# Kernel optimization log

Hardware: AMD Instinct MI355X
Metric: run time of the kernel (lower is better)

## Reference

```python
import jax, jax.numpy as jnp
import numpy as np

COUNTS = [1536, 8192, 16384, 24576, 12288, 1024, 512, 512, 256, 128, 128]
OFFS = np.concatenate([[0], np.cumsum(COUNTS)]).astype(int).tolist()
N = OFFS[-1]          # 65536 atoms total, sorted by degree
MAX_DEG = 10
BATCH = 2048          # fixed GraphGather batch size
F_IN = 75
GC = 256
DENSE = 512
N_TASKS = 12
N_CLASSES = 2
BN_EPS = 1e-3         # keras BatchNormalization default epsilon


def _graph_conv(x, deg_adjs, w0, wself, wneigh, b):
    # deepchem GraphConv: per-degree (self @ Wself + sum_neighbors @ Wneigh + b), relu
    outs = [x[OFFS[0]:OFFS[1]] @ w0 + b[0]]  # degree-0 atoms: self transform only
    for d in range(1, MAX_DEG + 1):
        self_atoms = x[OFFS[d]:OFFS[d + 1]]            # [n_d, F]
        neigh = x[deg_adjs[d - 1]].sum(axis=1)         # gather [n_d, d, F] -> sum -> [n_d, F]
        outs.append(self_atoms @ wself[d - 1] + neigh @ wneigh[d - 1] + b[d])
    return jax.nn.relu(jnp.concatenate(outs, axis=0))


def _graph_pool(x, deg_adjs):
    # deepchem GraphPool: elementwise max over {self} U neighbors, per degree
    outs = [x[OFFS[0]:OFFS[1]]]  # degree-0 atoms pass through
    for d in range(1, MAX_DEG + 1):
        self_atoms = x[OFFS[d]:OFFS[d + 1]]
        outs.append(jnp.maximum(self_atoms, x[deg_adjs[d - 1]].max(axis=1)))
    return jnp.concatenate(outs, axis=0)


def _bn(x, g, bta, m, v):
    # inference-mode BatchNormalization (training=False -> moving stats)
    return g * (x - m) * jax.lax.rsqrt(v + BN_EPS) + bta


def setup_inputs():
    key = jax.random.key(0)
    ks = iter(jax.random.split(key, 64))
    inp = {}
    inp["atom_features"] = jax.random.normal(next(ks), (N, F_IN), jnp.float32)
    inp["degree_slice"] = jnp.asarray(
        np.stack([np.array(OFFS[:-1]), np.array(COUNTS)], axis=1), jnp.int32)
    # each molecule gets exactly N/BATCH atoms so no GraphGather segment is empty
    inp["membership"] = jax.random.permutation(
        next(ks), jnp.arange(N, dtype=jnp.int32) % BATCH)
    inp["n_samples"] = BATCH
    for d in range(1, MAX_DEG + 1):
        inp["deg_adj_%d" % d] = jax.random.randint(
            next(ks), (COUNTS[d], d), 0, N, jnp.int32)

    def lin(k, fi, fo):
        return jax.random.normal(k, (fi, fo), jnp.float32) * np.float32(1.0 / np.sqrt(fi))

    for li, fi in [(1, F_IN), (2, GC)]:
        inp["gc%d_w0" % li] = lin(next(ks), fi, GC)
        inp["gc%d_wself" % li] = jnp.stack([lin(next(ks), fi, GC) for _ in range(MAX_DEG)])
        inp["gc%d_wneigh" % li] = jnp.stack([lin(next(ks), fi, GC) for _ in range(MAX_DEG)])
        inp["gc%d_b" % li] = jnp.zeros((MAX_DEG + 1, GC), jnp.float32)
    for bi, dim in [(1, GC), (2, GC), (3, DENSE)]:
        inp["bn%d_gamma" % bi] = jnp.ones((dim,), jnp.float32)
        inp["bn%d_beta" % bi] = jnp.zeros((dim,), jnp.float32)
        inp["bn%d_mean" % bi] = jnp.zeros((dim,), jnp.float32)
        inp["bn%d_var" % bi] = jnp.ones((dim,), jnp.float32)
    inp["dense_w"] = lin(next(ks), GC, DENSE)
    inp["dense_b"] = jnp.zeros((DENSE,), jnp.float32)
    inp["out_w"] = lin(next(ks), 2 * DENSE, N_TASKS * N_CLASSES)
    inp["out_b"] = jnp.zeros((N_TASKS * N_CLASSES,), jnp.float32)
    return inp


def reference(atom_features, degree_slice, membership, n_samples,
              deg_adj_1, deg_adj_2, deg_adj_3, deg_adj_4, deg_adj_5,
              deg_adj_6, deg_adj_7, deg_adj_8, deg_adj_9, deg_adj_10,
              gc1_w0, gc1_wself, gc1_wneigh, gc1_b,
              gc2_w0, gc2_wself, gc2_wneigh, gc2_b,
              bn1_gamma, bn1_beta, bn1_mean, bn1_var,
              bn2_gamma, bn2_beta, bn2_mean, bn2_var,
              bn3_gamma, bn3_beta, bn3_mean, bn3_var,
              dense_w, dense_b, out_w, out_b):
    deg_adjs = [deg_adj_1, deg_adj_2, deg_adj_3, deg_adj_4, deg_adj_5,
                deg_adj_6, deg_adj_7, deg_adj_8, deg_adj_9, deg_adj_10]
    h = _graph_conv(atom_features, deg_adjs, gc1_w0, gc1_wself, gc1_wneigh, gc1_b)
    h = _bn(h, bn1_gamma, bn1_beta, bn1_mean, bn1_var)
    h = _graph_pool(h, deg_adjs)
    h = _graph_conv(h, deg_adjs, gc2_w0, gc2_wself, gc2_wneigh, gc2_b)
    h = _bn(h, bn2_gamma, bn2_beta, bn2_mean, bn2_var)
    h = _graph_pool(h, deg_adjs)
    h = jax.nn.relu(h @ dense_w + dense_b)
    h = _bn(h, bn3_gamma, bn3_beta, bn3_mean, bn3_var)
    # GraphGather: tanh(concat(segment_sum, segment_max))
    ssum = jax.ops.segment_sum(h, membership, num_segments=BATCH)
    smax = jax.ops.segment_max(h, membership, num_segments=BATCH)
    fp = jnp.tanh(jnp.concatenate([ssum, smax], axis=1))   # [BATCH, 2*DENSE]
    logits = (fp @ out_w + out_b).reshape(BATCH, N_TASKS, N_CLASSES)[:n_samples]
    probs = jax.nn.softmax(logits, axis=-1)
    return probs, logits, fp
```

## Files before the change

kernel.cpp:

```cpp
#include <hip/hip_runtime.h>
#include <hip/hip_fp16.h>
#include <math.h>

#define NATOMS 65536

typedef _Float16 f16_t;
typedef __attribute__((ext_vector_type(8))) _Float16 half8;
typedef __attribute__((ext_vector_type(4))) float f32x4;

__constant__ int c_offs[12] = {0,1536,9728,26112,50688,62976,64000,64512,65024,65280,65408,65536};

struct Adj { const int* p[10]; };

__device__ __forceinline__ int seg_of(int row) {
    int s = 0;
#pragma unroll
    for (int i = 1; i <= 10; ++i) s += (row >= c_offs[i]) ? 1 : 0;
    return s;
}

__device__ __forceinline__ void glds16(const f16_t* g, f16_t* l) {
    __builtin_amdgcn_global_load_lds(
        (const __attribute__((address_space(1))) unsigned int*)g,
        (__attribute__((address_space(3))) unsigned int*)l,
        16, 0, 0);
}


__global__ void pack_w1(const float* __restrict__ w0, const float* __restrict__ wself,
                        const float* __restrict__ wneigh, f16_t* __restrict__ Wp) {
    int idx = blockIdx.x * 256 + threadIdx.x;
    int j = idx & 7, lane = (idx >> 3) & 63;
    int kb = (idx >> 9) % 6;
    int rest = idx / (512 * 6);
    int ni = rest & 15, s = rest >> 4;
    int k = kb * 32 + (lane >> 4) * 8 + j;
    int n = ni * 16 + (lane & 15);
    float v = 0.f;
    if (k < 75) v = (s == 0) ? w0[k*256 + n] : wself[((s-1)*75 + k)*256 + n];
    else if (k >= 96 && k < 171 && s > 0) v = wneigh[((s-1)*75 + (k-96))*256 + n];
    Wp[idx] = (f16_t)v;
}

__global__ void pack_w2(const float* __restrict__ w0, const float* __restrict__ wself,
                        const float* __restrict__ wneigh, f16_t* __restrict__ Wp) {
    int idx = blockIdx.x * 256 + threadIdx.x;
    int j = idx & 7, lane = (idx >> 3) & 63;
    int kb = (idx >> 9) & 15;
    int rest = idx >> 13;
    int ni = rest & 15, s = rest >> 4;
    int k = kb * 32 + (lane >> 4) * 8 + j;
    int n = ni * 16 + (lane & 15);
    float v = 0.f;
    if (k < 256) v = (s == 0) ? w0[k*256 + n] : wself[((s-1)*256 + k)*256 + n];
    else if (s > 0) v = wneigh[((s-1)*256 + (k-256))*256 + n];
    Wp[idx] = (f16_t)v;
}

__global__ void pack_wd(const float* __restrict__ w, f16_t* __restrict__ Wp) {
    int idx = blockIdx.x * 256 + threadIdx.x;
    int j = idx & 7, lane = (idx >> 3) & 63;
    int kb = (idx >> 9) & 7;
    int ni = (idx >> 12) & 31;
    int k = kb * 32 + (lane >> 4) * 8 + j;
    int n = ni * 16 + (lane & 15);
    Wp[idx] = (f16_t)w[(size_t)k*512 + n];
}

__global__ void pack_wo(const float* __restrict__ w, f16_t* __restrict__ Wp) {
    int idx = blockIdx.x * 256 + threadIdx.x;
    int j = idx & 7, lane = (idx >> 3) & 63;
    int kb = (idx >> 9) & 31;
    int ni = idx >> 14;
    int k = kb * 32 + (lane >> 4) * 8 + j;
    int n = ni * 16 + (lane & 15);
    Wp[idx] = (n < 24) ? (f16_t)w[k*24 + n] : (f16_t)0.f;
}

__global__ void cvt_pad(const float* __restrict__ xf, f16_t* __restrict__ xq) {
    int idx = blockIdx.x * 256 + threadIdx.x;
    int r = idx / 96;
    int c = idx - r * 96;
    xq[idx] = (c < 75) ? (f16_t)xf[(size_t)r*75 + c] : (f16_t)0.f;
}

template<int D, bool ISMAX, int LD>
__device__ __forceinline__ void gathD(float* v, const f16_t* __restrict__ src,
                                      const int* __restrict__ ap, int c) {
    int rows[D];
#pragma unroll
    for (int j = 0; j < D; ++j) rows[j] = ap[j];
    uint4 raw[D];
#pragma unroll
    for (int j = 0; j < D; ++j) raw[j] = *(const uint4*)(src + (size_t)rows[j]*LD + c);
#pragma unroll
    for (int j = 0; j < D; ++j) {
        const f16_t* u = (const f16_t*)&raw[j];
#pragma unroll
        for (int e = 0; e < 8; ++e) {
            float f = (float)u[e];
            v[e] = ISMAX ? fmaxf(v[e], f) : (v[e] + f);
        }
    }
}

template<bool ISMAX, int LD>
__device__ __forceinline__ void gath_switch(float* v, const f16_t* __restrict__ src,
                                            const int* __restrict__ ap, int s, int c) {
    switch (s) {
        case 1:  gathD<1,ISMAX,LD>(v,src,ap,c);  break;
        case 2:  gathD<2,ISMAX,LD>(v,src,ap,c);  break;
        case 3:  gathD<3,ISMAX,LD>(v,src,ap,c);  break;
        case 4:  gathD<4,ISMAX,LD>(v,src,ap,c);  break;
        case 5:  gathD<5,ISMAX,LD>(v,src,ap,c);  break;
        case 6:  gathD<6,ISMAX,LD>(v,src,ap,c);  break;
        case 7:  gathD<7,ISMAX,LD>(v,src,ap,c);  break;
        case 8:  gathD<8,ISMAX,LD>(v,src,ap,c);  break;
        case 9:  gathD<9,ISMAX,LD>(v,src,ap,c);  break;
        case 10: gathD<10,ISMAX,LD>(v,src,ap,c); break;
        default: break;
    }
}

__global__ __launch_bounds__(256) void nbsum_x(const f16_t* __restrict__ xq, f16_t* __restrict__ NBX, Adj adj) {
    int idx = blockIdx.x * 256 + threadIdx.x;
    int r = idx >> 4;
    int cc = idx & 15;
    if (cc >= 12) return;
    int c = cc << 3;
    int s = seg_of(r);
    float v[8];
#pragma unroll
    for (int e = 0; e < 8; ++e) v[e] = 0.f;
    if (s > 0)
        gath_switch<false,96>(v, xq, adj.p[s-1] + (size_t)(r - c_offs[s]) * s, s, c);
    f16_t o[8];
#pragma unroll
    for (int e = 0; e < 8; ++e) o[e] = (f16_t)v[e];
    *(uint4*)(NBX + (size_t)r*96 + c) = *(uint4*)o;
}

__global__ __launch_bounds__(256) void pool_k(const f16_t* __restrict__ H, f16_t* __restrict__ P, Adj adj) {
    int idx = blockIdx.x * 256 + threadIdx.x;
    int r = idx >> 5;
    int c = (idx & 31) << 3;
    int s = seg_of(r);
    uint4 self = *(const uint4*)(H + (size_t)r*256 + c);
    const f16_t* hp = (const f16_t*)&self;
    float v[8];
#pragma unroll
    for (int e = 0; e < 8; ++e) v[e] = (float)hp[e];
    if (s > 0)
        gath_switch<true,256>(v, H, adj.p[s-1] + (size_t)(r - c_offs[s]) * s, s, c);
    f16_t o[8];
#pragma unroll
    for (int e = 0; e < 8; ++e) o[e] = (f16_t)v[e];
    *(uint4*)(P + (size_t)r*256 + c) = *(uint4*)o;
}

__global__ __launch_bounds__(256) void nbsum_k(const f16_t* __restrict__ P, f16_t* __restrict__ NB, Adj adj) {
    int idx = blockIdx.x * 256 + threadIdx.x;
    int r = idx >> 5;
    int c = (idx & 31) << 3;
    int s = seg_of(r);
    float v[8];
#pragma unroll
    for (int e = 0; e < 8; ++e) v[e] = 0.f;
    if (s > 0)
        gath_switch<false,256>(v, P, adj.p[s-1] + (size_t)(r - c_offs[s]) * s, s, c);
    f16_t o[8];
#pragma unroll
    for (int e = 0; e < 8; ++e) o[e] = (f16_t)v[e];
    *(uint4*)(NB + (size_t)r*256 + c) = *(uint4*)o;
}

template<int K, int KSPLIT, int LDA, int N, int NY, bool SEG>
__global__ __launch_bounds__(256)
void gemm_mfma(const f16_t* __restrict__ A0, const f16_t* __restrict__ A1,
               const f16_t* __restrict__ Wp,
               const float* __restrict__ bias,
               const float* __restrict__ bng, const float* __restrict__ bnb,
               const float* __restrict__ bnm, const float* __restrict__ bnv,
               f16_t* __restrict__ C)
{
    constexpr int NKB = K / 32;
    constexpr int NNT = N / 16;
    __shared__ char smem[32768];
    f16_t* sm = (f16_t*)smem;
    f16_t* eps = (f16_t*)smem;

    const int t = threadIdx.x;
    const int lane = t & 63, wave = t >> 6;
    const int wm = wave >> 1, wn = wave & 1;
    const int quad = lane >> 4, l16 = lane & 15;
    const int id = blockIdx.x;
    const int xcd = id & 7;
    const int jj = id >> 3;
    const int xi = jj / NY;
    const int y  = jj - xi * NY;
    const int r0 = (xi * 8 + xcd) * 128;
    const int n0 = y * 128;
    const int seg = SEG ? seg_of(r0) : 0;
    const int nbase = n0 >> 4;

    f32x4 acc[4][4];
#pragma unroll
    for (int mi = 0; mi < 4; ++mi)
#pragma unroll
        for (int ni = 0; ni < 4; ++ni) acc[mi][ni] = (f32x4){0.f,0.f,0.f,0.f};

    size_t aoff[2];
#pragma unroll
    for (int i = 0; i < 2; ++i)
        aoff[i] = (size_t)(r0 + (wave*2 + i)*16 + l16) * LDA + quad*8;
    size_t bbase[2];
#pragma unroll
    for (int i = 0; i < 2; ++i)
        bbase[i] = ((size_t)(seg*NNT + nbase + wave*2 + i) * NKB) * 512 + lane*8;

#pragma unroll
    for (int kbp = 0; kbp < NKB/2; ++kbp) {
#pragma unroll
        for (int u = 0; u < 2; ++u) {
            const int kb = kbp*2 + u;
            const int kg = kb * 32;
            const f16_t* Ab = (kg < KSPLIT) ? (A0 + kg) : (A1 + (kg - KSPLIT));
#pragma unroll
            for (int i = 0; i < 2; ++i) {
                glds16(Ab + aoff[i], sm + u*4096 + (wave*2 + i)*512);
                glds16(Wp + bbase[i] + (size_t)kb*512, sm + 8192 + u*4096 + (wave*2 + i)*512);
            }
        }
        __syncthreads();
#pragma unroll
        for (int u = 0; u < 2; ++u) {
            half8 a[4], b[4];
#pragma unroll
            for (int mi = 0; mi < 4; ++mi)
                a[mi] = *(const half8*)(sm + u*4096 + (wm*4 + mi)*512 + lane*8);
#pragma unroll
            for (int ni = 0; ni < 4; ++ni)
                b[ni] = *(const half8*)(sm + 8192 + u*4096 + (wn*4 + ni)*512 + lane*8);
#pragma unroll
            for (int mi = 0; mi < 4; ++mi)
#pragma unroll
                for (int ni = 0; ni < 4; ++ni)
                    acc[mi][ni] = __builtin_amdgcn_mfma_f32_16x16x32_f16(a[mi], b[ni], acc[mi][ni], 0, 0, 0);
        }
        __syncthreads();
    }

#pragma unroll
    for (int p = 0; p < 2; ++p) {
        if (wm == p) {
#pragma unroll
            for (int ni = 0; ni < 4; ++ni) {
                const int lcol = (wn*4 + ni)*16 + l16;
                const int col = n0 + lcol;
                const float scale = bng[col] * rsqrtf(bnv[col] + 1e-3f);
                const float shift = bnb[col] - bnm[col] * scale;
                const float bv = bias[(SEG ? seg*N : 0) + col];
#pragma unroll
                for (int mi = 0; mi < 4; ++mi) {
                    const int lrowb = mi*16 + quad*4;
#pragma unroll
                    for (int r = 0; r < 4; ++r) {
                        float v = acc[mi][ni][r] + bv;
                        v = fmaxf(v, 0.f);
                        v = fmaf(v, scale, shift);
                        eps[(lrowb + r)*136 + lcol] = (f16_t)v;
                    }
                }
            }
        }
        __syncthreads();
#pragma unroll
        for (int it = 0; it < 4; ++it) {
            int row = it*16 + (t >> 4);
            int ch  = t & 15;
            uint4 v = *(const uint4*)&eps[row*136 + ch*8];
            *(uint4*)(C + (size_t)(r0 + p*64 + row)*N + n0 + ch*8) = v;
        }
        __syncthreads();
    }
}

__global__ void scatter_k(const int* __restrict__ mem, int* __restrict__ counts, int* __restrict__ slots) {
    int i = blockIdx.x * 256 + threadIdx.x;
    int s = mem[i];
    int p = atomicAdd(&counts[s], 1);
    if (p < 32) slots[s*32 + p] = i;
}

__global__ __launch_bounds__(64)
void reduce_k(const f16_t* __restrict__ H3, const int* __restrict__ slots,
              float* __restrict__ fp, f16_t* __restrict__ fph) {
    int s = blockIdx.x, l = threadIdx.x;
    int c = l * 8;
    const int* sl = slots + s*32;
    float sm[8], mx[8];
#pragma unroll
    for (int e = 0; e < 8; ++e) { sm[e] = 0.f; mx[e] = -INFINITY; }
#pragma unroll
    for (int i = 0; i < 32; ++i) {
        int a = sl[i];
        uint4 raw = *(const uint4*)(H3 + (size_t)a*512 + c);
        const f16_t* u = (const f16_t*)&raw;
#pragma unroll
        for (int e = 0; e < 8; ++e) {
            float f = (float)u[e];
            sm[e] += f;
            mx[e] = fmaxf(mx[e], f);
        }
    }
    float o1[8], o2[8];
    f16_t h1[8], h2[8];
#pragma unroll
    for (int e = 0; e < 8; ++e) {
        o1[e] = tanhf(sm[e]); o2[e] = tanhf(mx[e]);
        h1[e] = (f16_t)o1[e]; h2[e] = (f16_t)o2[e];
    }
    float* fr = fp + (size_t)s*1024;
    *(float4*)(fr + c)       = *(float4*)&o1[0];
    *(float4*)(fr + c + 4)   = *(float4*)&o1[4];
    *(float4*)(fr + 512 + c)     = *(float4*)&o2[0];
    *(float4*)(fr + 512 + c + 4) = *(float4*)&o2[4];
    f16_t* fh = fph + (size_t)s*1024;
    *(uint4*)(fh + c)       = *(uint4*)h1;
    *(uint4*)(fh + 512 + c) = *(uint4*)h2;
}

__global__ __launch_bounds__(256)
void final_mfma(const f16_t* __restrict__ fph, const f16_t* __restrict__ Wop,
                const float* __restrict__ out_b,
                float* __restrict__ probs, float* __restrict__ logits) {
    const int t = threadIdx.x;
    const int lane = t & 63, wave = t >> 6;
    const int quad = lane >> 4, l16 = lane & 15;
    const int r0 = blockIdx.x * 256 + wave * 64;

    f32x4 acc[4][2];
#pragma unroll
    for (int mi = 0; mi < 4; ++mi)
#pragma unroll
        for (int ni = 0; ni < 2; ++ni) acc[mi][ni] = (f32x4){0.f,0.f,0.f,0.f};

    size_t rowoff[4];
#pragma unroll
    for (int mi = 0; mi < 4; ++mi)
        rowoff[mi] = (size_t)(r0 + mi*16 + l16) * 1024 + quad*8;
    size_t boff[2];
#pragma unroll
    for (int ni = 0; ni < 2; ++ni)
        boff[ni] = (size_t)ni * 32 * 512 + lane*8;

    auto loadA = [&](half8* a, int kb) {
#pragma unroll
        for (int mi = 0; mi < 4; ++mi) a[mi] = *(const half8*)(fph + rowoff[mi] + kb*32);
    };
    auto loadB = [&](half8* b, int kb) {
#pragma unroll
        for (int ni = 0; ni < 2; ++ni) b[ni] = *(const half8*)(Wop + boff[ni] + (size_t)kb*512);
    };
    auto domfma = [&](half8* a, half8* b) {
#pragma unroll
        for (int mi = 0; mi < 4; ++mi)
#pragma unroll
            for (int ni = 0; ni < 2; ++ni)
                acc[mi][ni] = __builtin_amdgcn_mfma_f32_16x16x32_f16(a[mi], b[ni], acc[mi][ni], 0, 0, 0);
    };

    half8 a0[4], b0[2], a1[4], b1[2];
    loadA(a0, 0); loadB(b0, 0);
#pragma unroll
    for (int kb = 0; kb < 32; kb += 2) {
        loadA(a1, kb + 1); loadB(b1, kb + 1);
        domfma(a0, b0);
        if (kb + 2 < 32) { loadA(a0, kb + 2); loadB(b0, kb + 2); }
        domfma(a1, b1);
    }

#pragma unroll
    for (int ni = 0; ni < 2; ++ni) {
        const int c = ni*16 + l16;
        const bool ok = (c < 24);
        const float bv = ok ? out_b[c] : 0.f;
#pragma unroll
        for (int mi = 0; mi < 4; ++mi) {
#pragma unroll
            for (int r = 0; r < 4; ++r) {
                float lg = acc[mi][ni][r] + bv;
                float lp = __shfl_xor(lg, 1);
                float m = fmaxf(lg, lp);
                float e  = expf(lg - m);
                float ep = expf(lp - m);
                float pr = e / (e + ep);
                if (ok) {
                    int row = r0 + mi*16 + quad*4 + r;
                    logits[(size_t)row*24 + c] = lg;
                    probs[(size_t)row*24 + c]  = pr;
                }
            }
        }
    }
}

extern "C" void kernel_launch(void* const* d_in, const int* in_sizes, int n_in,
                              void* d_out, int out_size, void* d_ws, size_t ws_size,
                              hipStream_t stream) {
    const float* atom       = (const float*)d_in[0];
    const int*   membership = (const int*)  d_in[2];
    Adj adj;
    for (int d = 0; d < 10; ++d) adj.p[d] = (const int*)d_in[4+d];
    const float* gc1_w0     = (const float*)d_in[14];
    const float* gc1_wself  = (const float*)d_in[15];
    const float* gc1_wneigh = (const float*)d_in[16];
    const float* gc1_b      = (const float*)d_in[17];
    const float* gc2_w0     = (const float*)d_in[18];
    const float* gc2_wself  = (const float*)d_in[19];
    const float* gc2_wneigh = (const float*)d_in[20];
    const float* gc2_b      = (const float*)d_in[21];
    const float* bn1g = (const float*)d_in[22]; const float* bn1b = (const float*)d_in[23];
    const float* bn1m = (const float*)d_in[24]; const float* bn1v = (const float*)d_in[25];
    const float* bn2g = (const float*)d_in[26]; const float* bn2b = (const float*)d_in[27];
    const float* bn2m = (const float*)d_in[28]; const float* bn2v = (const float*)d_in[29];
    const float* bn3g = (const float*)d_in[30]; const float* bn3b = (const float*)d_in[31];
    const float* bn3m = (const float*)d_in[32]; const float* bn3v = (const float*)d_in[33];
    const float* dense_w = (const float*)d_in[34];
    const float* dense_b = (const float*)d_in[35];
    const float* out_w   = (const float*)d_in[36];
    const float* out_b   = (const float*)d_in[37];

    f16_t* wsb = (f16_t*)d_ws;
    f16_t* xq   = wsb;
    f16_t* NBX  = wsb + 6291456;
    f16_t* H1b  = wsb + 12582912;
    f16_t* P1b  = wsb + 29360128;
    f16_t* NB2b = wsb + 46137344;
    f16_t* H2b  = H1b;
    f16_t* P2b  = NB2b;
    f16_t* H3b  = H1b;
    f16_t* W1p  = wsb + 62914560;
    f16_t* W2p  = wsb + 63455232;
    f16_t* Wdp  = wsb + 64897024;
    f16_t* fph  = wsb + 65028096;
    f16_t* Wop  = wsb + 67125248;
    int*  counts = (int*)(wsb + 67158016);
    int*  slots  = counts + 2048;

    float* outp   = (float*)d_out;
    float* probs  = outp;
    float* logits = outp + 49152;
    float* fp     = outp + 98304;

    pack_w1<<<2112, 256, 0, stream>>>(gc1_w0, gc1_wself, gc1_wneigh, W1p);
    pack_w2<<<5632, 256, 0, stream>>>(gc2_w0, gc2_wself, gc2_wneigh, W2p);
    pack_wd<<<512,  256, 0, stream>>>(dense_w, Wdp);
    pack_wo<<<128,  256, 0, stream>>>(out_w, Wop);

    cvt_pad<<<(NATOMS*96)/256, 256, 0, stream>>>(atom, xq);
    nbsum_x<<<(NATOMS*16)/256, 256, 0, stream>>>(xq, NBX, adj);
    gemm_mfma<192,96,96,256,2,true><<<1024, 256, 0, stream>>>(
        xq, NBX, W1p, gc1_b, bn1g, bn1b, bn1m, bn1v, H1b);
    pool_k<<<(NATOMS*32)/256, 256, 0, stream>>>(H1b, P1b, adj);

    nbsum_k<<<(NATOMS*32)/256, 256, 0, stream>>>(P1b, NB2b, adj);
    gemm_mfma<512,256,256,256,2,true><<<1024, 256, 0, stream>>>(
        P1b, NB2b, W2p, gc2_b, bn2g, bn2b, bn2m, bn2v, H2b);
    pool_k<<<(NATOMS*32)/256, 256, 0, stream>>>(H2b, P2b, adj);

    gemm_mfma<256,256,256,512,4,false><<<2048, 256, 0, stream>>>(
        P2b, P2b, Wdp, dense_b, bn3g, bn3b, bn3m, bn3v, H3b);

    hipMemsetAsync((void*)counts, 0, 2048*sizeof(int), stream);
    scatter_k<<<NATOMS/256, 256, 0, stream>>>(membership, counts, slots);
    reduce_k<<<2048, 64, 0, stream>>>(H3b, slots, fp, fph);

    final_mfma<<<8, 256, 0, stream>>>(fph, Wop, out_b, probs, logits);
}
```

Baseline: 383.8 us.

## Store activations in MFMA-fragment tiled layout so GEMM A loads are contiguous

Activation buffers (xq, NBX, H, P, NB, H3) switch from row-major to a 16-row × 32-column tiled layout that matches the MFMA fragment order used by the GEMM. GEMM A-operand global-to-LDS loads become fully contiguous 1KB chunks, and the epilogue writes out in the same tiled order. The gather, pool, reduce and cvt kernels are rewritten to address the tiled layout, so each neighbor gather of 16 bytes now lands in a row-block-strided location. This reduces strided row accesses in the GEMMs, but gathers may lose some locality within rows.

```diff
diff --git a/kernel.cpp b/kernel.cpp
--- a/kernel.cpp
+++ b/kernel.cpp
@@ -25,6 +25,7 @@
         (__attribute__((address_space(3))) unsigned int*)l,
         16, 0, 0);
 }
+
 
 
 __global__ void pack_w1(const float* __restrict__ w0, const float* __restrict__ wself,
@@ -79,20 +80,29 @@
 
 __global__ void cvt_pad(const float* __restrict__ xf, f16_t* __restrict__ xq) {
     int idx = blockIdx.x * 256 + threadIdx.x;
-    int r = idx / 96;
-    int c = idx - r * 96;
-    xq[idx] = (c < 75) ? (f16_t)xf[(size_t)r*75 + c] : (f16_t)0.f;
-}
-
-template<int D, bool ISMAX, int LD>
+    int r = idx / 12;
+    int cc = idx - r * 12;
+    int c = cc << 3;
+    f16_t o[8];
+#pragma unroll
+    for (int e = 0; e < 8; ++e)
+        o[e] = (c + e < 75) ? (f16_t)xf[(size_t)r*75 + c + e] : (f16_t)0.f;
+    f16_t* dst = xq + (size_t)(r>>4)*1536 + (c>>5)*512 + ((c>>3)&3)*128 + (r&15)*8;
+    *(uint4*)dst = *(uint4*)o;
+}
+
+template<int D, bool ISMAX>
 __device__ __forceinline__ void gathD(float* v, const f16_t* __restrict__ src,
-                                      const int* __restrict__ ap, int c) {
+                                      const int* __restrict__ ap, int rsb, int off) {
     int rows[D];
 #pragma unroll
     for (int j = 0; j < D; ++j) rows[j] = ap[j];
     uint4 raw[D];
 #pragma unroll
-    for (int j = 0; j < D; ++j) raw[j] = *(const uint4*)(src + (size_t)rows[j]*LD + c);
+    for (int j = 0; j < D; ++j) {
+        int a = rows[j];
+        raw[j] = *(const uint4*)(src + (size_t)(a>>4)*rsb + off + (a&15)*8);
+    }
 #pragma unroll
     for (int j = 0; j < D; ++j) {
         const f16_t* u = (const f16_t*)&raw[j];
@@ -104,20 +114,20 @@
     }
 }
 
-template<bool ISMAX, int LD>
+template<bool ISMAX>
 __device__ __forceinline__ void gath_switch(float* v, const f16_t* __restrict__ src,
-                                            const int* __restrict__ ap, int s, int c) {
+                                            const int* __restrict__ ap, int s, int rsb, int off) {
     switch (s) {
-        case 1:  gathD<1,ISMAX,LD>(v,src,ap,c);  break;
-        case 2:  gathD<2,ISMAX,LD>(v,src,ap,c);  break;
-        case 3:  gathD<3,ISMAX,LD>(v,src,ap,c);  break;
-        case 4:  gathD<4,ISMAX,LD>(v,src,ap,c);  break;
-        case 5:  gathD<5,ISMAX,LD>(v,src,ap,c);  break;
-        case 6:  gathD<6,ISMAX,LD>(v,src,ap,c);  break;
-        case 7:  gathD<7,ISMAX,LD>(v,src,ap,c);  break;
-        case 8:  gathD<8,ISMAX,LD>(v,src,ap,c);  break;
-        case 9:  gathD<9,ISMAX,LD>(v,src,ap,c);  break;
-        case 10: gathD<10,ISMAX,LD>(v,src,ap,c); break;
+        case 1:  gathD<1,ISMAX>(v,src,ap,rsb,off);  break;
+        case 2:  gathD<2,ISMAX>(v,src,ap,rsb,off);  break;
+        case 3:  gathD<3,ISMAX>(v,src,ap,rsb,off);  break;
+        case 4:  gathD<4,ISMAX>(v,src,ap,rsb,off);  break;
+        case 5:  gathD<5,ISMAX>(v,src,ap,rsb,off);  break;
+        case 6:  gathD<6,ISMAX>(v,src,ap,rsb,off);  break;
+        case 7:  gathD<7,ISMAX>(v,src,ap,rsb,off);  break;
+        case 8:  gathD<8,ISMAX>(v,src,ap,rsb,off);  break;
+        case 9:  gathD<9,ISMAX>(v,src,ap,rsb,off);  break;
+        case 10: gathD<10,ISMAX>(v,src,ap,rsb,off); break;
         default: break;
     }
 }
@@ -128,53 +138,56 @@
     int cc = idx & 15;
     if (cc >= 12) return;
     int c = cc << 3;
+    int off = (c>>5)*512 + ((c>>3)&3)*128;
     int s = seg_of(r);
     float v[8];
 #pragma unroll
     for (int e = 0; e < 8; ++e) v[e] = 0.f;
     if (s > 0)
-        gath_switch<false,96>(v, xq, adj.p[s-1] + (size_t)(r - c_offs[s]) * s, s, c);
+        gath_switch<false>(v, xq, adj.p[s-1] + (size_t)(r - c_offs[s]) * s, s, 1536, off);
     f16_t o[8];
 #pragma unroll
     for (int e = 0; e < 8; ++e) o[e] = (f16_t)v[e];
-    *(uint4*)(NBX + (size_t)r*96 + c) = *(uint4*)o;
+    *(uint4*)(NBX + (size_t)(r>>4)*1536 + off + (r&15)*8) = *(uint4*)o;
 }
 
 __global__ __launch_bounds__(256) void pool_k(const f16_t* __restrict__ H, f16_t* __restrict__ P, Adj adj) {
     int idx = blockIdx.x * 256 + threadIdx.x;
     int r = idx >> 5;
     int c = (idx & 31) << 3;
+    int off = (c>>5)*512 + ((c>>3)&3)*128;
     int s = seg_of(r);
-    uint4 self = *(const uint4*)(H + (size_t)r*256 + c);
+    uint4 self = *(const uint4*)(H + (size_t)(r>>4)*4096 + off + (r&15)*8);
     const f16_t* hp = (const f16_t*)&self;
     float v[8];
 #pragma unroll
     for (int e = 0; e < 8; ++e) v[e] = (float)hp[e];
     if (s > 0)
-        gath_switch<true,256>(v, H, adj.p[s-1] + (size_t)(r - c_offs[s]) * s, s, c);
+        gath_switch<true>(v, H, adj.p[s-1] + (size_t)(r - c_offs[s]) * s, s, 4096, off);
     f16_t o[8];
 #pragma unroll
     for (int e = 0; e < 8; ++e) o[e] = (f16_t)v[e];
-    *(uint4*)(P + (size_t)r*256 + c) = *(uint4*)o;
+    *(uint4*)(P + (size_t)(r>>4)*4096 + off + (r&15)*8) = *(uint4*)o;
 }
 
 __global__ __launch_bounds__(256) void nbsum_k(const f16_t* __restrict__ P, f16_t* __restrict__ NB, Adj adj) {
     int idx = blockIdx.x * 256 + threadIdx.x;
     int r = idx >> 5;
     int c = (idx & 31) << 3;
+    int off = (c>>5)*512 + ((c>>3)&3)*128;
     int s = seg_of(r);
     float v[8];
 #pragma unroll
     for (int e = 0; e < 8; ++e) v[e] = 0.f;
     if (s > 0)
-        gath_switch<false,256>(v, P, adj.p[s-1] + (size_t)(r - c_offs[s]) * s, s, c);
+        gath_switch<false>(v, P, adj.p[s-1] + (size_t)(r - c_offs[s]) * s, s, 4096, off);
     f16_t o[8];
 #pragma unroll
     for (int e = 0; e < 8; ++e) o[e] = (f16_t)v[e];
-    *(uint4*)(NB + (size_t)r*256 + c) = *(uint4*)o;
-}
-
-template<int K, int KSPLIT, int LDA, int N, int NY, bool SEG>
+    *(uint4*)(NB + (size_t)(r>>4)*4096 + off + (r&15)*8) = *(uint4*)o;
+}
+
+template<int NKB, int KSPB, int NKBA0, int NKBA1, int N, int NKBC, int NY, bool SEG>
 __global__ __launch_bounds__(256)
 void gemm_mfma(const f16_t* __restrict__ A0, const f16_t* __restrict__ A1,
                const f16_t* __restrict__ Wp,
@@ -183,7 +196,6 @@
                const float* __restrict__ bnm, const float* __restrict__ bnv,
                f16_t* __restrict__ C)
 {
-    constexpr int NKB = K / 32;
     constexpr int NNT = N / 16;
     __shared__ char smem[32768];
     f16_t* sm = (f16_t*)smem;
@@ -202,33 +214,28 @@
     const int n0 = y * 128;
     const int seg = SEG ? seg_of(r0) : 0;
     const int nbase = n0 >> 4;
+    const int rtg = r0 >> 4;
 
     f32x4 acc[4][4];
 #pragma unroll
     for (int mi = 0; mi < 4; ++mi)
 #pragma unroll
         for (int ni = 0; ni < 4; ++ni) acc[mi][ni] = (f32x4){0.f,0.f,0.f,0.f};
-
-    size_t aoff[2];
-#pragma unroll
-    for (int i = 0; i < 2; ++i)
-        aoff[i] = (size_t)(r0 + (wave*2 + i)*16 + l16) * LDA + quad*8;
-    size_t bbase[2];
-#pragma unroll
-    for (int i = 0; i < 2; ++i)
-        bbase[i] = ((size_t)(seg*NNT + nbase + wave*2 + i) * NKB) * 512 + lane*8;
 
 #pragma unroll
     for (int kbp = 0; kbp < NKB/2; ++kbp) {
 #pragma unroll
         for (int u = 0; u < 2; ++u) {
             const int kb = kbp*2 + u;
-            const int kg = kb * 32;
-            const f16_t* Ab = (kg < KSPLIT) ? (A0 + kg) : (A1 + (kg - KSPLIT));
 #pragma unroll
             for (int i = 0; i < 2; ++i) {
-                glds16(Ab + aoff[i], sm + u*4096 + (wave*2 + i)*512);
-                glds16(Wp + bbase[i] + (size_t)kb*512, sm + 8192 + u*4096 + (wave*2 + i)*512);
+                const int rt = wave*2 + i;
+                const f16_t* asrc = (kb < KSPB)
+                    ? A0 + ((size_t)(rtg + rt)*NKBA0 + kb)*512
+                    : A1 + ((size_t)(rtg + rt)*NKBA1 + (kb - KSPB))*512;
+                glds16(asrc + lane*8, sm + u*4096 + rt*512);
+                glds16(Wp + ((size_t)(seg*NNT + nbase + rt)*NKB + kb)*512 + lane*8,
+                       sm + 8192 + u*4096 + rt*512);
             }
         }
         __syncthreads();
@@ -276,10 +283,12 @@
         __syncthreads();
 #pragma unroll
         for (int it = 0; it < 4; ++it) {
-            int row = it*16 + (t >> 4);
-            int ch  = t & 15;
-            uint4 v = *(const uint4*)&eps[row*136 + ch*8];
-            *(uint4*)(C + (size_t)(r0 + p*64 + row)*N + n0 + ch*8) = v;
+            const int bi = it*4 + wave;
+            const int rt = bi >> 2;
+            const int kbl = bi & 3;
+            uint4 v = *(const uint4*)(eps + (rt*16 + l16)*136 + kbl*32 + quad*8);
+            f16_t* dst = C + ((size_t)(rtg + p*4 + rt)*NKBC + (n0>>5) + kbl)*512 + lane*8;
+            *(uint4*)dst = v;
         }
         __syncthreads();
     }
@@ -297,6 +306,7 @@
               float* __restrict__ fp, f16_t* __restrict__ fph) {
     int s = blockIdx.x, l = threadIdx.x;
     int c = l * 8;
+    int off = (c>>5)*512 + ((c>>3)&3)*128;
     const int* sl = slots + s*32;
     float sm[8], mx[8];
 #pragma unroll
@@ -304,7 +314,7 @@
 #pragma unroll
     for (int i = 0; i < 32; ++i) {
         int a = sl[i];
-        uint4 raw = *(const uint4*)(H3 + (size_t)a*512 + c);
+        uint4 raw = *(const uint4*)(H3 + (size_t)(a>>4)*8192 + off + (a&15)*8);
         const f16_t* u = (const f16_t*)&raw;
 #pragma unroll
         for (int e = 0; e < 8; ++e) {
@@ -458,18 +468,18 @@
     pack_wd<<<512,  256, 0, stream>>>(dense_w, Wdp);
     pack_wo<<<128,  256, 0, stream>>>(out_w, Wop);
 
-    cvt_pad<<<(NATOMS*96)/256, 256, 0, stream>>>(atom, xq);
+    cvt_pad<<<(NATOMS*12)/256, 256, 0, stream>>>(atom, xq);
     nbsum_x<<<(NATOMS*16)/256, 256, 0, stream>>>(xq, NBX, adj);
-    gemm_mfma<192,96,96,256,2,true><<<1024, 256, 0, stream>>>(
+    gemm_mfma<6,3,3,3,256,8,2,true><<<1024, 256, 0, stream>>>(
         xq, NBX, W1p, gc1_b, bn1g, bn1b, bn1m, bn1v, H1b);
     pool_k<<<(NATOMS*32)/256, 256, 0, stream>>>(H1b, P1b, adj);
 
     nbsum_k<<<(NATOMS*32)/256, 256, 0, stream>>>(P1b, NB2b, adj);
-    gemm_mfma<512,256,256,256,2,true><<<1024, 256, 0, stream>>>(
+    gemm_mfma<16,8,8,8,256,8,2,true><<<1024, 256, 0, stream>>>(
         P1b, NB2b, W2p, gc2_b, bn2g, bn2b, bn2m, bn2v, H2b);
     pool_k<<<(NATOMS*32)/256, 256, 0, stream>>>(H2b, P2b, adj);
 
-    gemm_mfma<256,256,256,512,4,false><<<2048, 256, 0, stream>>>(
+    gemm_mfma<8,8,8,8,512,16,4,false><<<2048, 256, 0, stream>>>(
         P2b, P2b, Wdp, dense_b, bn3g, bn3b, bn3m, bn3v, H3b);
 
     hipMemsetAsync((void*)counts, 0, 2048*sizeof(int), stream);
```

Result: slower. 678.0 us (+76.7%).

## Store GEMM A operands in MFMA-blocked tile layout for contiguous LDS loads

Applied to the files above, without the earlier changes.

Producer kernels (cvt_pad, nbsum, pool) now write their outputs in a blocked 16-row x 32-col tile layout, so each wave's global_load_lds in the GEMM reads one contiguous 1 KB chunk instead of 16 strided row segments. Where later gathers still need row-major access, pool_k writes both a blocked and a row-major copy. cvt_pad is also vectorised to 8 elements per thread. In exchange there is extra write traffic for the dual copy, scattered 16-byte stores in the producers, and a larger workspace.

```diff
diff --git a/kernel.cpp b/kernel.cpp
--- a/kernel.cpp
+++ b/kernel.cpp
@@ -77,11 +77,18 @@
     Wp[idx] = (n < 24) ? (f16_t)w[k*24 + n] : (f16_t)0.f;
 }
 
-__global__ void cvt_pad(const float* __restrict__ xf, f16_t* __restrict__ xq) {
-    int idx = blockIdx.x * 256 + threadIdx.x;
-    int r = idx / 96;
-    int c = idx - r * 96;
-    xq[idx] = (c < 75) ? (f16_t)xf[(size_t)r*75 + c] : (f16_t)0.f;
+__global__ void cvt_pad(const float* __restrict__ xf,
+                        f16_t* __restrict__ xq_rm, f16_t* __restrict__ xq_bl) {
+    int idx = blockIdx.x * 256 + threadIdx.x;
+    int r = idx / 12;
+    int cc = idx - r * 12;
+    int c = cc << 3;
+    f16_t o[8];
+#pragma unroll
+    for (int e = 0; e < 8; ++e)
+        o[e] = (c + e < 75) ? (f16_t)xf[(size_t)r*75 + c + e] : (f16_t)0.f;
+    *(uint4*)(xq_rm + (size_t)r*96 + c) = *(uint4*)o;
+    *(uint4*)(xq_bl + (size_t)(r>>4)*1536 + (c>>5)*512 + ((c>>3)&3)*128 + (r&15)*8) = *(uint4*)o;
 }
 
 template<int D, bool ISMAX, int LD>
@@ -122,7 +129,8 @@
     }
 }
 
-__global__ __launch_bounds__(256) void nbsum_x(const f16_t* __restrict__ xq, f16_t* __restrict__ NBX, Adj adj) {
+__global__ __launch_bounds__(256) void nbsum_x(const f16_t* __restrict__ xq_rm,
+                                               f16_t* __restrict__ NBX, Adj adj) {
     int idx = blockIdx.x * 256 + threadIdx.x;
     int r = idx >> 4;
     int cc = idx & 15;
@@ -133,14 +141,17 @@
 #pragma unroll
     for (int e = 0; e < 8; ++e) v[e] = 0.f;
     if (s > 0)
-        gath_switch<false,96>(v, xq, adj.p[s-1] + (size_t)(r - c_offs[s]) * s, s, c);
+        gath_switch<false,96>(v, xq_rm, adj.p[s-1] + (size_t)(r - c_offs[s]) * s, s, c);
     f16_t o[8];
 #pragma unroll
     for (int e = 0; e < 8; ++e) o[e] = (f16_t)v[e];
-    *(uint4*)(NBX + (size_t)r*96 + c) = *(uint4*)o;
-}
-
-__global__ __launch_bounds__(256) void pool_k(const f16_t* __restrict__ H, f16_t* __restrict__ P, Adj adj) {
+    *(uint4*)(NBX + (size_t)(r>>4)*1536 + (c>>5)*512 + ((c>>3)&3)*128 + (r&15)*8) = *(uint4*)o;
+}
+
+template<bool DUAL>
+__global__ __launch_bounds__(256) void pool_k(const f16_t* __restrict__ H,
+                                              f16_t* __restrict__ P_bl,
+                                              f16_t* __restrict__ P_rm, Adj adj) {
     int idx = blockIdx.x * 256 + threadIdx.x;
     int r = idx >> 5;
     int c = (idx & 31) << 3;
@@ -155,10 +166,13 @@
     f16_t o[8];
 #pragma unroll
     for (int e = 0; e < 8; ++e) o[e] = (f16_t)v[e];
-    *(uint4*)(P + (size_t)r*256 + c) = *(uint4*)o;
-}
-
-__global__ __launch_bounds__(256) void nbsum_k(const f16_t* __restrict__ P, f16_t* __restrict__ NB, Adj adj) {
+    *(uint4*)(P_bl + (size_t)(r>>4)*4096 + (c>>5)*512 + ((c>>3)&3)*128 + (r&15)*8) = *(uint4*)o;
+    if (DUAL)
+        *(uint4*)(P_rm + (size_t)r*256 + c) = *(uint4*)o;
+}
+
+__global__ __launch_bounds__(256) void nbsum_k(const f16_t* __restrict__ P_rm,
+                                               f16_t* __restrict__ NB, Adj adj) {
     int idx = blockIdx.x * 256 + threadIdx.x;
     int r = idx >> 5;
     int c = (idx & 31) << 3;
@@ -167,14 +181,14 @@
 #pragma unroll
     for (int e = 0; e < 8; ++e) v[e] = 0.f;
     if (s > 0)
-        gath_switch<false,256>(v, P, adj.p[s-1] + (size_t)(r - c_offs[s]) * s, s, c);
+        gath_switch<false,256>(v, P_rm, adj.p[s-1] + (size_t)(r - c_offs[s]) * s, s, c);
     f16_t o[8];
 #pragma unroll
     for (int e = 0; e < 8; ++e) o[e] = (f16_t)v[e];
-    *(uint4*)(NB + (size_t)r*256 + c) = *(uint4*)o;
-}
-
-template<int K, int KSPLIT, int LDA, int N, int NY, bool SEG>
+    *(uint4*)(NB + (size_t)(r>>4)*4096 + (c>>5)*512 + ((c>>3)&3)*128 + (r&15)*8) = *(uint4*)o;
+}
+
+template<int NKB, int KSPB, int NKBA0, int NKBA1, int N, int NY, bool SEG>
 __global__ __launch_bounds__(256)
 void gemm_mfma(const f16_t* __restrict__ A0, const f16_t* __restrict__ A1,
                const f16_t* __restrict__ Wp,
@@ -183,7 +197,6 @@
                const float* __restrict__ bnm, const float* __restrict__ bnv,
                f16_t* __restrict__ C)
 {
-    constexpr int NKB = K / 32;
     constexpr int NNT = N / 16;
     __shared__ char smem[32768];
     f16_t* sm = (f16_t*)smem;
@@ -202,33 +215,28 @@
     const int n0 = y * 128;
     const int seg = SEG ? seg_of(r0) : 0;
     const int nbase = n0 >> 4;
+    const int rtg = r0 >> 4;
 
     f32x4 acc[4][4];
 #pragma unroll
     for (int mi = 0; mi < 4; ++mi)
 #pragma unroll
         for (int ni = 0; ni < 4; ++ni) acc[mi][ni] = (f32x4){0.f,0.f,0.f,0.f};
-
-    size_t aoff[2];
-#pragma unroll
-    for (int i = 0; i < 2; ++i)
-        aoff[i] = (size_t)(r0 + (wave*2 + i)*16 + l16) * LDA + quad*8;
-    size_t bbase[2];
-#pragma unroll
-    for (int i = 0; i < 2; ++i)
-        bbase[i] = ((size_t)(seg*NNT + nbase + wave*2 + i) * NKB) * 512 + lane*8;
 
 #pragma unroll
     for (int kbp = 0; kbp < NKB/2; ++kbp) {
 #pragma unroll
         for (int u = 0; u < 2; ++u) {
             const int kb = kbp*2 + u;
-            const int kg = kb * 32;
-            const f16_t* Ab = (kg < KSPLIT) ? (A0 + kg) : (A1 + (kg - KSPLIT));
 #pragma unroll
             for (int i = 0; i < 2; ++i) {
-                glds16(Ab + aoff[i], sm + u*4096 + (wave*2 + i)*512);
-                glds16(Wp + bbase[i] + (size_t)kb*512, sm + 8192 + u*4096 + (wave*2 + i)*512);
+                const int rt = wave*2 + i;
+                const f16_t* asrc = (kb < KSPB)
+                    ? A0 + ((size_t)(rtg + rt)*NKBA0 + kb)*512
+                    : A1 + ((size_t)(rtg + rt)*NKBA1 + (kb - KSPB))*512;
+                glds16(asrc + lane*8, sm + u*4096 + rt*512);
+                glds16(Wp + ((size_t)(seg*NNT + nbase + rt)*NKB + kb)*512 + lane*8,
+                       sm + 8192 + u*4096 + rt*512);
             }
         }
         __syncthreads();
@@ -432,20 +440,22 @@
     const float* out_b   = (const float*)d_in[37];
 
     f16_t* wsb = (f16_t*)d_ws;
-    f16_t* xq   = wsb;
-    f16_t* NBX  = wsb + 6291456;
-    f16_t* H1b  = wsb + 12582912;
-    f16_t* P1b  = wsb + 29360128;
-    f16_t* NB2b = wsb + 46137344;
-    f16_t* H2b  = H1b;
-    f16_t* P2b  = NB2b;
-    f16_t* H3b  = H1b;
-    f16_t* W1p  = wsb + 62914560;
-    f16_t* W2p  = wsb + 63455232;
-    f16_t* Wdp  = wsb + 64897024;
-    f16_t* fph  = wsb + 65028096;
-    f16_t* Wop  = wsb + 67125248;
-    int*  counts = (int*)(wsb + 67158016);
+    f16_t* xq_rm = wsb;
+    f16_t* xq_bl = wsb + 6291456;
+    f16_t* NBX   = wsb + 12582912;
+    f16_t* H1b   = wsb + 18874368;
+    f16_t* P1rm  = wsb + 35651584;
+    f16_t* P1bl  = wsb + 52428800;
+    f16_t* NB2b  = wsb + 69206016;
+    f16_t* H2b   = H1b;
+    f16_t* P2bl  = NB2b;
+    f16_t* H3b   = wsb + 35651584;
+    f16_t* W1p   = wsb + 85983232;
+    f16_t* W2p   = wsb + 86523904;
+    f16_t* Wdp   = wsb + 87965696;
+    f16_t* Wop   = wsb + 88096768;
+    f16_t* fph   = wsb + 88129536;
+    int*  counts = (int*)(wsb + 90226688);
     int*  slots  = counts + 2048;
 
     float* outp   = (float*)d_out;
@@ -458,19 +468,19 @@
     pack_wd<<<512,  256, 0, stream>>>(dense_w, Wdp);
     pack_wo<<<128,  256, 0, stream>>>(out_w, Wop);
 
-    cvt_pad<<<(NATOMS*96)/256, 256, 0, stream>>>(atom, xq);
-    nbsum_x<<<(NATOMS*16)/256, 256, 0, stream>>>(xq, NBX, adj);
-    gemm_mfma<192,96,96,256,2,true><<<1024, 256, 0, stream>>>(
-        xq, NBX, W1p, gc1_b, bn1g, bn1b, bn1m, bn1v, H1b);
-    pool_k<<<(NATOMS*32)/256, 256, 0, stream>>>(H1b, P1b, adj);
-
-    nbsum_k<<<(NATOMS*32)/256, 256, 0, stream>>>(P1b, NB2b, adj);
-    gemm_mfma<512,256,256,256,2,true><<<1024, 256, 0, stream>>>(
-        P1b, NB2b, W2p, gc2_b, bn2g, bn2b, bn2m, bn2v, H2b);
-    pool_k<<<(NATOMS*32)/256, 256, 0, stream>>>(H2b, P2b, adj);
-
-    gemm_mfma<256,256,256,512,4,false><<<2048, 256, 0, stream>>>(
-        P2b, P2b, Wdp, dense_b, bn3g, bn3b, bn3m, bn3v, H3b);
+    cvt_pad<<<(NATOMS*12)/256, 256, 0, stream>>>(atom, xq_rm, xq_bl);
+    nbsum_x<<<(NATOMS*16)/256, 256, 0, stream>>>(xq_rm, NBX, adj);
+    gemm_mfma<6,3,3,3,256,2,true><<<1024, 256, 0, stream>>>(
+        xq_bl, NBX, W1p, gc1_b, bn1g, bn1b, bn1m, bn1v, H1b);
+    pool_k<true><<<(NATOMS*32)/256, 256, 0, stream>>>(H1b, P1bl, P1rm, adj);
+
+    nbsum_k<<<(NATOMS*32)/256, 256, 0, stream>>>(P1rm, NB2b, adj);
+    gemm_mfma<16,8,8,8,256,2,true><<<1024, 256, 0, stream>>>(
+        P1bl, NB2b, W2p, gc2_b, bn2g, bn2b, bn2m, bn2v, H2b);
+    pool_k<false><<<(NATOMS*32)/256, 256, 0, stream>>>(H2b, P2bl, nullptr, adj);
+
+    gemm_mfma<8,8,8,8,512,4,false><<<2048, 256, 0, stream>>>(
+        P2bl, P2bl, Wdp, dense_b, bn3g, bn3b, bn3m, bn3v, H3b);
 
     hipMemsetAsync((void*)counts, 0, 2048*sizeof(int), stream);
     scatter_k<<<NATOMS/256, 256, 0, stream>>>(membership, counts, slots);
```

After: 387.1 us. About the same (+0.9%).
